# Optimization experiments

Measured on AMD Instinct MI355X. Metric: run time of the kernel, lower is better.

Reference implementation:

```python
import jax, jax.numpy as jnp
import numpy as np

N = 100000      # nodes
E = 1600000     # directed edges
LAT = 128
MAT = 8
OUT = 3


def setup_inputs() -> dict:
    key = jax.random.key(0)
    ks = jax.random.split(key, 5)
    z = jax.random.normal(ks[0], (N, LAT), dtype=jnp.float32)
    material_params = jax.random.normal(ks[1], (N, MAT), dtype=jnp.float32)
    edge_index = jax.random.randint(ks[2], (2, E), 0, N, dtype=jnp.int64)
    W1 = jax.random.normal(ks[3], (LAT + MAT, LAT), dtype=jnp.float32) * 0.05
    b1 = jnp.zeros((LAT,), dtype=jnp.float32)
    W2 = jax.random.normal(ks[4], (LAT, OUT), dtype=jnp.float32) * 0.05
    b2 = jnp.zeros((OUT,), dtype=jnp.float32)
    return {"z": z, "edge_index": edge_index, "material_params": material_params,
            "W1": W1, "b1": b1, "W2": W2, "b2": b2}


def _gcn_norm(edge_index, num_nodes):
    # PyG GCNConv default: add self-loops, symmetric normalization
    src, dst = edge_index[0], edge_index[1]
    loop = jnp.arange(num_nodes, dtype=src.dtype)
    row = jnp.concatenate([src, loop])  # message source
    col = jnp.concatenate([dst, loop])  # message target
    deg = jax.ops.segment_sum(jnp.ones_like(col, dtype=jnp.float32), col,
                              num_segments=num_nodes)
    dinv = jnp.where(deg > 0, jax.lax.rsqrt(deg), 0.0)
    norm = dinv[row] * dinv[col]        # [E + N]
    return row, col, norm


def _gcn_conv(x, W, b, row, col, norm, num_nodes):
    h = x @ W                                   # linear first (PyG order)
    msg = h[row] * norm[:, None]                # gather + scale
    agg = jax.ops.segment_sum(msg, col, num_segments=num_nodes)
    return agg + b


def reference(z, edge_index, material_params, W1, b1, W2, b2):
    row, col, norm = _gcn_norm(edge_index, N)
    x = jnp.concatenate([z, material_params], axis=1)     # [N, LAT+MAT]
    x = jax.nn.relu(_gcn_conv(x, W1, b1, row, col, norm, N))
    x = _gcn_conv(x, W2, b2, row, col, norm, N)           # [N, OUT]
    return x
```

## Files before the change

### kernel.cpp

```cpp
#include <hip/hip_runtime.h>

#define N_NODES 100000
#define N_EDGES 1600000
#define LAT 128
#define MAT 8
#define OUTC 3

#define NBKT 391
#define CAP  4608
#define CHUNK 4096

typedef __attribute__((ext_vector_type(8))) short bf16x8;
typedef __attribute__((ext_vector_type(4))) float f32x4;

__device__ __forceinline__ unsigned short bf16r(float f) {
    unsigned int u = __float_as_uint(f);
    u = (u + 0x7fffu + ((u >> 16) & 1u)) >> 16;
    return (unsigned short)u;
}
__device__ __forceinline__ float bf16f(unsigned short h) {
    return __uint_as_float((unsigned int)h << 16);
}
__device__ __forceinline__ unsigned int pack_bf16(float a, float b) {
    return (unsigned int)bf16r(a) | ((unsigned int)bf16r(b) << 16);
}

__global__ __launch_bounds__(256) void k_binA(const int* __restrict__ src,
                                              const int* __restrict__ dst,
                                              int* __restrict__ gcount,
                                              unsigned int* __restrict__ binned) {
    __shared__ int hist[NBKT];
    __shared__ int adj[NBKT];
    __shared__ int cur[NBKT];
    __shared__ int wsum[4];
    __shared__ unsigned int lbuf[CHUNK];
    __shared__ unsigned short lbkt[CHUNK];

    int t = threadIdx.x;
    int base = blockIdx.x * CHUNK;
    int nEdge = min(CHUNK, N_EDGES - base);

    for (int i = t; i < NBKT; i += 256) hist[i] = 0;
    __syncthreads();

    unsigned int pk[16];
    unsigned short bk[16];
#pragma unroll
    for (int j = 0; j < 16; ++j) {
        int li = j * 256 + t;
        if (li < nEdge) {
            int e = base + li;
            int d = dst[e];
            int s = src[e];
            pk[j] = ((unsigned int)s << 8) | (unsigned int)(d & 255);
            bk[j] = (unsigned short)(d >> 8);
            atomicAdd(&hist[bk[j]], 1);
        } else {
            bk[j] = 0xffffu;
        }
    }
    __syncthreads();

    int lane = t & 63, w = t >> 6;
    int i0 = 2 * t, i1 = 2 * t + 1;
    int h0 = (i0 < NBKT) ? hist[i0] : 0;
    int h1 = (i1 < NBKT) ? hist[i1] : 0;
    int ps = h0 + h1;
    int x = ps;
#pragma unroll
    for (int off = 1; off < 64; off <<= 1) {
        int y = __shfl_up(x, off, 64);
        if (lane >= off) x += y;
    }
    if (lane == 63) wsum[w] = x;
    __syncthreads();
    int woff = 0;
#pragma unroll
    for (int i = 0; i < 4; ++i)
        if (i < w) woff += wsum[i];
    int excl = woff + x - ps;
    if (i0 < NBKT) {
        int g0 = i0 * CAP + atomicAdd(&gcount[i0], h0);
        adj[i0] = g0 - excl;
        cur[i0] = excl;
    }
    if (i1 < NBKT) {
        int g1r = i1 * CAP + atomicAdd(&gcount[i1], h1);
        adj[i1] = g1r - (excl + h0);
        cur[i1] = excl + h0;
    }
    __syncthreads();

#pragma unroll
    for (int j = 0; j < 16; ++j) {
        if (bk[j] != 0xffffu) {
            int pos = atomicAdd(&cur[bk[j]], 1);
            lbuf[pos] = pk[j];
            lbkt[pos] = bk[j];
        }
    }
    __syncthreads();

    for (int i = t; i < nEdge; i += 256) {
        int b = lbkt[i];
        binned[adj[b] + i] = lbuf[i];
    }
}

__global__ __launch_bounds__(256) void k_bscan(const int* __restrict__ gcount,
                                               int* __restrict__ bucketBase,
                                               int* __restrict__ rowptr) {
    __shared__ int wsum[4];
    int t = threadIdx.x;
    int lane = t & 63, w = t >> 6;
    int i0 = 2 * t, i1 = 2 * t + 1;
    int h0 = (i0 < NBKT) ? gcount[i0] : 0;
    int h1 = (i1 < NBKT) ? gcount[i1] : 0;
    int ps = h0 + h1;
    int x = ps;
#pragma unroll
    for (int off = 1; off < 64; off <<= 1) {
        int y = __shfl_up(x, off, 64);
        if (lane >= off) x += y;
    }
    if (lane == 63) wsum[w] = x;
    __syncthreads();
    int woff = 0;
#pragma unroll
    for (int i = 0; i < 4; ++i)
        if (i < w) woff += wsum[i];
    int excl = woff + x - ps;
    bucketBase[i0] = excl;
    bucketBase[i1] = excl + h0;
    if (t == 0) rowptr[N_NODES] = N_EDGES;
}

__global__ __launch_bounds__(256) void k_binB(const unsigned int* __restrict__ binned,
                                              const int* __restrict__ gcount,
                                              const int* __restrict__ bucketBase,
                                              int* __restrict__ colsrc,
                                              int* __restrict__ rowptr,
                                              float* __restrict__ dinv) {
    __shared__ unsigned int lbuf[CAP];
    __shared__ int lsrc[CAP];
    __shared__ int hist[256];
    __shared__ int cur[256];
    __shared__ int wsum[4];

    int b = blockIdx.x, t = threadIdx.x;
    int cnt = min(gcount[b], CAP);
    int gb = bucketBase[b];
    const unsigned int* bp = binned + (size_t)b * CAP;

    for (int i = t; i < cnt; i += 256) lbuf[i] = bp[i];
    hist[t] = 0;
    __syncthreads();
    for (int i = t; i < cnt; i += 256) atomicAdd(&hist[lbuf[i] & 255], 1);
    __syncthreads();

    int lane = t & 63, w = t >> 6;
    int h = hist[t];
    int x = h;
#pragma unroll
    for (int off = 1; off < 64; off <<= 1) {
        int y = __shfl_up(x, off, 64);
        if (lane >= off) x += y;
    }
    if (lane == 63) wsum[w] = x;
    __syncthreads();
    int woff = 0;
#pragma unroll
    for (int i = 0; i < 4; ++i)
        if (i < w) woff += wsum[i];
    int excl = woff + x - h;
    cur[t] = excl;

    int node = b * 256 + t;
    if (node < N_NODES) {
        rowptr[node] = gb + excl;
        dinv[node] = rsqrtf((float)h + 1.0f);
    }
    __syncthreads();

    for (int i = t; i < cnt; i += 256) {
        unsigned int p = lbuf[i];
        int pos = atomicAdd(&cur[p & 255], 1);
        lsrc[pos] = (int)(p >> 8);
    }
    __syncthreads();

    for (int i = t; i < cnt; i += 256) colsrc[gb + i] = lsrc[i];
}

__global__ void k_wsplit(const float* __restrict__ W1,
                         unsigned short* __restrict__ w1h,
                         unsigned short* __restrict__ w1l) {
    int i = blockIdx.x * 256 + threadIdx.x;
    if (i >= 160 * 128) return;
    int k = i >> 7;
    float w = (k < LAT + MAT) ? W1[i] : 0.f;
    unsigned short h = bf16r(w);
    w1h[i] = h;
    w1l[i] = bf16r(w - bf16f(h));
}

__global__ __launch_bounds__(256) void k_gemm1m(const float* __restrict__ z,
                                                const float* __restrict__ mat,
                                                const unsigned short* __restrict__ w1h,
                                                const unsigned short* __restrict__ w1l,
                                                const float* __restrict__ dinv,
                                                unsigned short* __restrict__ g1h) {
    int wv = threadIdx.x >> 6;
    int l = threadIdx.x & 63;
    int lm = l & 15, q = l >> 4;

    bf16x8 bh[2][5], bl[2][5];
#pragma unroll
    for (int ct = 0; ct < 2; ++ct) {
        int col = (wv * 2 + ct) * 16 + lm;
#pragma unroll
        for (int ks = 0; ks < 5; ++ks) {
#pragma unroll
            for (int j = 0; j < 8; ++j) {
                int k = ks * 32 + q * 8 + j;
                bh[ct][ks][j] = (short)w1h[k * 128 + col];
                bl[ct][ks][j] = (short)w1l[k * 128 + col];
            }
        }
    }

    for (int tile = blockIdx.x; tile < N_NODES / 16; tile += gridDim.x) {
        int n0 = tile * 16;
        int row = n0 + lm;
        f32x4 acc0 = {0.f, 0.f, 0.f, 0.f};
        f32x4 acc1 = {0.f, 0.f, 0.f, 0.f};
#pragma unroll
        for (int ks = 0; ks < 5; ++ks) {
            float a[8];
            if (ks < 4) {
                float4 a0 = *(const float4*)&z[(size_t)row * LAT + ks * 32 + q * 8];
                float4 a1 = *(const float4*)&z[(size_t)row * LAT + ks * 32 + q * 8 + 4];
                a[0] = a0.x; a[1] = a0.y; a[2] = a0.z; a[3] = a0.w;
                a[4] = a1.x; a[5] = a1.y; a[6] = a1.z; a[7] = a1.w;
            } else if (q == 0) {
                float4 m0 = *(const float4*)&mat[(size_t)row * MAT];
                float4 m1 = *(const float4*)&mat[(size_t)row * MAT + 4];
                a[0] = m0.x; a[1] = m0.y; a[2] = m0.z; a[3] = m0.w;
                a[4] = m1.x; a[5] = m1.y; a[6] = m1.z; a[7] = m1.w;
            } else {
#pragma unroll
                for (int j = 0; j < 8; ++j) a[j] = 0.f;
            }
            bf16x8 ah, al;
#pragma unroll
            for (int j = 0; j < 8; ++j) {
                unsigned short h = bf16r(a[j]);
                ah[j] = (short)h;
                al[j] = (short)bf16r(a[j] - bf16f(h));
            }
            acc0 = __builtin_amdgcn_mfma_f32_16x16x32_bf16(ah, bh[0][ks], acc0, 0, 0, 0);
            acc1 = __builtin_amdgcn_mfma_f32_16x16x32_bf16(ah, bh[1][ks], acc1, 0, 0, 0);
            acc0 = __builtin_amdgcn_mfma_f32_16x16x32_bf16(al, bh[0][ks], acc0, 0, 0, 0);
            acc1 = __builtin_amdgcn_mfma_f32_16x16x32_bf16(al, bh[1][ks], acc1, 0, 0, 0);
            acc0 = __builtin_amdgcn_mfma_f32_16x16x32_bf16(ah, bl[0][ks], acc0, 0, 0, 0);
            acc1 = __builtin_amdgcn_mfma_f32_16x16x32_bf16(ah, bl[1][ks], acc1, 0, 0, 0);
        }
#pragma unroll
        for (int r = 0; r < 4; ++r) {
            int m = q * 4 + r;
            float d = dinv[n0 + m];
            g1h[(size_t)(n0 + m) * 128 + (wv * 2 + 0) * 16 + lm] = bf16r(acc0[r] * d);
            g1h[(size_t)(n0 + m) * 128 + (wv * 2 + 1) * 16 + lm] = bf16r(acc1[r] * d);
        }
    }
}

__global__ __launch_bounds__(256) void k_gather1(const unsigned int* __restrict__ g1h,
                                                 const int* __restrict__ colsrc,
                                                 const int* __restrict__ rowptr,
                                                 const float* __restrict__ dinv,
                                                 const float* __restrict__ b1,
                                                 const float* __restrict__ W2,
                                                 float* __restrict__ g2) {
    int n = blockIdx.x * 4 + (threadIdx.x >> 6);
    int lane = threadIdx.x & 63;
    unsigned int au = g1h[(size_t)n * 64 + lane];
    float ax = __uint_as_float(au << 16);
    float ay = __uint_as_float(au & 0xffff0000u);
    int e0 = rowptr[n], eEnd = rowptr[n + 1];
    for (int e = e0; e < eEnd; e += 16) {
        unsigned int u[16];
#pragma unroll
        for (int j = 0; j < 16; ++j) {
            int idx = e + j;
            bool valid = idx < eEnd;
            int cs = colsrc[valid ? idx : e0];
            int s = valid ? cs : n;
            u[j] = g1h[(size_t)s * 64 + lane];
            if (!valid) u[j] = 0;
        }
#pragma unroll
        for (int j = 0; j < 16; ++j) {
            ax += __uint_as_float(u[j] << 16);
            ay += __uint_as_float(u[j] & 0xffff0000u);
        }
    }
    float d = dinv[n];
    float2 bb = ((const float2*)b1)[lane];
    float x0 = fmaxf(ax * d + bb.x, 0.f);
    float x1 = fmaxf(ay * d + bb.y, 0.f);
    float p0 = x0 * W2[(2 * lane) * OUTC + 0] + x1 * W2[(2 * lane + 1) * OUTC + 0];
    float p1 = x0 * W2[(2 * lane) * OUTC + 1] + x1 * W2[(2 * lane + 1) * OUTC + 1];
    float p2 = x0 * W2[(2 * lane) * OUTC + 2] + x1 * W2[(2 * lane + 1) * OUTC + 2];
#pragma unroll
    for (int off = 32; off > 0; off >>= 1) {
        p0 += __shfl_down(p0, off, 64);
        p1 += __shfl_down(p1, off, 64);
        p2 += __shfl_down(p2, off, 64);
    }
    if (lane == 0) ((float4*)g2)[n] = make_float4(p0 * d, p1 * d, p2 * d, 0.f);
}

__global__ void k_gather2(const float* __restrict__ g2, const int* __restrict__ colsrc,
                          const int* __restrict__ rowptr, const float* __restrict__ dinv,
                          const float* __restrict__ b2, float* __restrict__ out) {
    int n = blockIdx.x * blockDim.x + threadIdx.x;
    if (n >= N_NODES) return;
    const float4* gv = (const float4*)g2;
    float4 a = gv[n];
    float s0 = a.x, s1 = a.y, s2 = a.z;
    int eEnd = rowptr[n + 1];
    for (int e = rowptr[n]; e < eEnd; ++e) {
        float4 v = gv[colsrc[e]];
        s0 += v.x; s1 += v.y; s2 += v.z;
    }
    float d = dinv[n];
    out[(size_t)n * 3 + 0] = s0 * d + b2[0];
    out[(size_t)n * 3 + 1] = s1 * d + b2[1];
    out[(size_t)n * 3 + 2] = s2 * d + b2[2];
}


extern "C" void kernel_launch(void* const* d_in, const int* in_sizes, int n_in,
                              void* d_out, int out_size, void* d_ws, size_t ws_size,
                              hipStream_t stream) {
    const float* z   = (const float*)d_in[0];
    const int*   ei  = (const int*)d_in[1];
    const float* mat = (const float*)d_in[2];
    const float* W1  = (const float*)d_in[3];
    const float* b1  = (const float*)d_in[4];
    const float* W2  = (const float*)d_in[5];
    const float* b2  = (const float*)d_in[6];
    float* out = (float*)d_out;

    const int* srcA = ei;
    const int* dstA = ei + N_EDGES;

    char* ws = (char*)d_ws;
    auto alloc = [&](size_t bytes) {
        char* p = ws;
        ws += (bytes + 255) & ~(size_t)255;
        return p;
    };
    int*   gcount     = (int*)alloc(512 * 4);
    int*   bucketBase = (int*)alloc(512 * 4);
    int*   rowptr     = (int*)alloc((size_t)(N_NODES + 1) * 4);
    float* dinv       = (float*)alloc((size_t)N_NODES * 4);
    int*   colsrc     = (int*)alloc((size_t)N_EDGES * 4);
    unsigned int* g1h = (unsigned int*)alloc((size_t)N_NODES * 64 * 4);
    float* g2         = (float*)alloc((size_t)N_NODES * 4 * 4);
    unsigned short* w1h = (unsigned short*)alloc(160 * 128 * 2);
    unsigned short* w1l = (unsigned short*)alloc(160 * 128 * 2);
    unsigned int* binned = g1h;

    hipMemsetAsync(gcount, 0, 512 * 4, stream);
    int nBlocksA = (N_EDGES + CHUNK - 1) / CHUNK;
    k_binA<<<nBlocksA, 256, 0, stream>>>(srcA, dstA, gcount, binned);
    k_bscan<<<1, 256, 0, stream>>>(gcount, bucketBase, rowptr);
    k_binB<<<NBKT, 256, 0, stream>>>(binned, gcount, bucketBase, colsrc, rowptr, dinv);
    k_wsplit<<<(160 * 128 + 255) / 256, 256, 0, stream>>>(W1, w1h, w1l);
    k_gemm1m<<<1250, 256, 0, stream>>>(z, mat, w1h, w1l, dinv, (unsigned short*)g1h);
    k_gather1<<<N_NODES / 4, 256, 0, stream>>>(g1h, colsrc, rowptr, dinv, b1, W2, g2);
    k_gather2<<<(N_NODES + 255) / 256, 256, 0, stream>>>(g2, colsrc, rowptr, dinv, b2, out);
}
```

Baseline: 168.1 us.

## Partition hidden features into 8 column slabs for cache-local gather

The GEMM output is stored as 8 column slabs of 16 bf16 features per node instead of one 128-wide row. The first aggregation now runs one block per node and slab, with 8 edges processed in parallel per wave, so each pass touches a 3.2MB slab that can stay in cache. Partial W2 projections are written per slab and summed by a new reduction kernel. The cost is 8x more index reads of colsrc, an extra launch, and extra partial-sum traffic.

```diff
diff --git a/kernel.cpp b/kernel.cpp
--- a/kernel.cpp
+++ b/kernel.cpp
@@ -9,6 +9,7 @@
 #define NBKT 391
 #define CAP  4608
 #define CHUNK 4096
+#define NPART 8
 
 typedef __attribute__((ext_vector_type(8))) short bf16x8;
 typedef __attribute__((ext_vector_type(4))) float f32x4;
@@ -20,9 +21,6 @@
 }
 __device__ __forceinline__ float bf16f(unsigned short h) {
     return __uint_as_float((unsigned int)h << 16);
-}
-__device__ __forceinline__ unsigned int pack_bf16(float a, float b) {
-    return (unsigned int)bf16r(a) | ((unsigned int)bf16r(b) << 16);
 }
 
 __global__ __launch_bounds__(256) void k_binA(const int* __restrict__ src,
@@ -209,7 +207,7 @@
                                                 const unsigned short* __restrict__ w1h,
                                                 const unsigned short* __restrict__ w1l,
                                                 const float* __restrict__ dinv,
-                                                unsigned short* __restrict__ g1h) {
+                                                unsigned short* __restrict__ g1p) {
     int wv = threadIdx.x >> 6;
     int l = threadIdx.x & 63;
     int lm = l & 15, q = l >> 4;
@@ -269,56 +267,77 @@
         for (int r = 0; r < 4; ++r) {
             int m = q * 4 + r;
             float d = dinv[n0 + m];
-            g1h[(size_t)(n0 + m) * 128 + (wv * 2 + 0) * 16 + lm] = bf16r(acc0[r] * d);
-            g1h[(size_t)(n0 + m) * 128 + (wv * 2 + 1) * 16 + lm] = bf16r(acc1[r] * d);
+            g1p[(size_t)(wv * 2 + 0) * (N_NODES * 16) + (size_t)(n0 + m) * 16 + lm] = bf16r(acc0[r] * d);
+            g1p[(size_t)(wv * 2 + 1) * (N_NODES * 16) + (size_t)(n0 + m) * 16 + lm] = bf16r(acc1[r] * d);
         }
     }
 }
 
-__global__ __launch_bounds__(256) void k_gather1(const unsigned int* __restrict__ g1h,
-                                                 const int* __restrict__ colsrc,
-                                                 const int* __restrict__ rowptr,
-                                                 const float* __restrict__ dinv,
-                                                 const float* __restrict__ b1,
-                                                 const float* __restrict__ W2,
-                                                 float* __restrict__ g2) {
-    int n = blockIdx.x * 4 + (threadIdx.x >> 6);
-    int lane = threadIdx.x & 63;
-    unsigned int au = g1h[(size_t)n * 64 + lane];
-    float ax = __uint_as_float(au << 16);
-    float ay = __uint_as_float(au & 0xffff0000u);
+__global__ __launch_bounds__(256) void k_gather1p(const unsigned int* __restrict__ g1p,
+                                                  const int* __restrict__ colsrc,
+                                                  const int* __restrict__ rowptr,
+                                                  const float* __restrict__ dinv,
+                                                  const float* __restrict__ b1,
+                                                  const float* __restrict__ W2,
+                                                  float4* __restrict__ pp) {
+    int p = blockIdx.x & 7;
+    int nb = blockIdx.x >> 3;
+    int n = nb * 4 + (threadIdx.x >> 6);
+    int l = threadIdx.x & 63;
+    int c = l & 7;
+    int g = l >> 3;
+
+    const unsigned int* slab = g1p + (size_t)p * (N_NODES * 8);
+
+    unsigned int su = slab[(unsigned)n * 8u + c];
+    if (g != 0) su = 0u;
+    float ax = __uint_as_float(su << 16);
+    float ay = __uint_as_float(su & 0xffff0000u);
+
     int e0 = rowptr[n], eEnd = rowptr[n + 1];
-    for (int e = e0; e < eEnd; e += 16) {
-        unsigned int u[16];
-#pragma unroll
-        for (int j = 0; j < 16; ++j) {
-            int idx = e + j;
-            bool valid = idx < eEnd;
-            int cs = colsrc[valid ? idx : e0];
-            int s = valid ? cs : n;
-            u[j] = g1h[(size_t)s * 64 + lane];
-            if (!valid) u[j] = 0;
-        }
-#pragma unroll
-        for (int j = 0; j < 16; ++j) {
-            ax += __uint_as_float(u[j] << 16);
-            ay += __uint_as_float(u[j] & 0xffff0000u);
-        }
-    }
+    int nIt = (eEnd - e0 + 7) >> 3;
+    for (int it = 0; it < nIt; ++it) {
+        int idx = e0 + it * 8 + g;
+        bool v = idx < eEnd;
+        int s = v ? colsrc[v ? idx : e0] : n;
+        unsigned int u = slab[(unsigned)s * 8u + c];
+        if (!v) u = 0u;
+        ax += __uint_as_float(u << 16);
+        ay += __uint_as_float(u & 0xffff0000u);
+    }
+
+    ax += __shfl_xor(ax, 8, 64);  ay += __shfl_xor(ay, 8, 64);
+    ax += __shfl_xor(ax, 16, 64); ay += __shfl_xor(ay, 16, 64);
+    ax += __shfl_xor(ax, 32, 64); ay += __shfl_xor(ay, 32, 64);
+
     float d = dinv[n];
-    float2 bb = ((const float2*)b1)[lane];
+    int r = p * 16 + 2 * c;
+    float2 bb = *(const float2*)&b1[r];
     float x0 = fmaxf(ax * d + bb.x, 0.f);
     float x1 = fmaxf(ay * d + bb.y, 0.f);
-    float p0 = x0 * W2[(2 * lane) * OUTC + 0] + x1 * W2[(2 * lane + 1) * OUTC + 0];
-    float p1 = x0 * W2[(2 * lane) * OUTC + 1] + x1 * W2[(2 * lane + 1) * OUTC + 1];
-    float p2 = x0 * W2[(2 * lane) * OUTC + 2] + x1 * W2[(2 * lane + 1) * OUTC + 2];
-#pragma unroll
-    for (int off = 32; off > 0; off >>= 1) {
-        p0 += __shfl_down(p0, off, 64);
-        p1 += __shfl_down(p1, off, 64);
-        p2 += __shfl_down(p2, off, 64);
-    }
-    if (lane == 0) ((float4*)g2)[n] = make_float4(p0 * d, p1 * d, p2 * d, 0.f);
+    float p0 = x0 * W2[r * 3 + 0] + x1 * W2[r * 3 + 3];
+    float p1 = x0 * W2[r * 3 + 1] + x1 * W2[r * 3 + 4];
+    float p2 = x0 * W2[r * 3 + 2] + x1 * W2[r * 3 + 5];
+
+    p0 += __shfl_xor(p0, 1, 64); p1 += __shfl_xor(p1, 1, 64); p2 += __shfl_xor(p2, 1, 64);
+    p0 += __shfl_xor(p0, 2, 64); p1 += __shfl_xor(p1, 2, 64); p2 += __shfl_xor(p2, 2, 64);
+    p0 += __shfl_xor(p0, 4, 64); p1 += __shfl_xor(p1, 4, 64); p2 += __shfl_xor(p2, 4, 64);
+
+    if (l == 0) pp[(size_t)p * N_NODES + n] = make_float4(p0, p1, p2, 0.f);
+}
+
+__global__ void k_g2build(const float4* __restrict__ pp, const float* __restrict__ dinv,
+                          float4* __restrict__ g2) {
+    int n = blockIdx.x * blockDim.x + threadIdx.x;
+    if (n >= N_NODES) return;
+    float s0 = 0.f, s1 = 0.f, s2 = 0.f;
+#pragma unroll
+    for (int p = 0; p < NPART; ++p) {
+        float4 v = pp[(size_t)p * N_NODES + n];
+        s0 += v.x; s1 += v.y; s2 += v.z;
+    }
+    float d = dinv[n];
+    g2[n] = make_float4(s0 * d, s1 * d, s2 * d, 0.f);
 }
 
 __global__ void k_gather2(const float* __restrict__ g2, const int* __restrict__ colsrc,
@@ -367,11 +386,12 @@
     int*   rowptr     = (int*)alloc((size_t)(N_NODES + 1) * 4);
     float* dinv       = (float*)alloc((size_t)N_NODES * 4);
     int*   colsrc     = (int*)alloc((size_t)N_EDGES * 4);
-    unsigned int* g1h = (unsigned int*)alloc((size_t)N_NODES * 64 * 4);
+    unsigned short* g1p = (unsigned short*)alloc((size_t)NPART * N_NODES * 16 * 2);
+    float4* pp        = (float4*)alloc((size_t)NPART * N_NODES * 16);
     float* g2         = (float*)alloc((size_t)N_NODES * 4 * 4);
     unsigned short* w1h = (unsigned short*)alloc(160 * 128 * 2);
     unsigned short* w1l = (unsigned short*)alloc(160 * 128 * 2);
-    unsigned int* binned = g1h;
+    unsigned int* binned = (unsigned int*)g1p;
 
     hipMemsetAsync(gcount, 0, 512 * 4, stream);
     int nBlocksA = (N_EDGES + CHUNK - 1) / CHUNK;
@@ -379,7 +399,9 @@
     k_bscan<<<1, 256, 0, stream>>>(gcount, bucketBase, rowptr);
     k_binB<<<NBKT, 256, 0, stream>>>(binned, gcount, bucketBase, colsrc, rowptr, dinv);
     k_wsplit<<<(160 * 128 + 255) / 256, 256, 0, stream>>>(W1, w1h, w1l);
-    k_gemm1m<<<1250, 256, 0, stream>>>(z, mat, w1h, w1l, dinv, (unsigned short*)g1h);
-    k_gather1<<<N_NODES / 4, 256, 0, stream>>>(g1h, colsrc, rowptr, dinv, b1, W2, g2);
+    k_gemm1m<<<1250, 256, 0, stream>>>(z, mat, w1h, w1l, dinv, g1p);
+    k_gather1p<<<NPART * (N_NODES / 4), 256, 0, stream>>>((const unsigned int*)g1p, colsrc,
+                                                          rowptr, dinv, b1, W2, pp);
+    k_g2build<<<(N_NODES + 255) / 256, 256, 0, stream>>>(pp, dinv, (float4*)g2);
     k_gather2<<<(N_NODES + 255) / 256, 256, 0, stream>>>(g2, colsrc, rowptr, dinv, b2, out);
 }
```

New measurement: 357.9 us. 2.13x slower.
